# Kernel optimization log

Hardware: AMD Instinct MI355X
Metric: run time of the kernel (lower is better)

Reference implementation:

```python
import jax, jax.numpy as jnp
import numpy as np

H = 128          # hidden_size
D = 128          # input_size
N_LEAVES = 262144  # 2**18 leaves -> complete binary tree, 18 reduction levels


def setup_inputs() -> dict:
    key = jax.random.key(0)
    k1, k2, k3, k4, k5 = jax.random.split(key, 5)
    s = 0.05
    return {
        "leaf_features": jax.random.normal(k1, (N_LEAVES, D), jnp.float32),
        "W_x": jax.random.normal(k2, (D, 5 * H), jnp.float32) * s,  # torch Linear weight (transposed)
        "b_x": jax.random.normal(k3, (5 * H,), jnp.float32) * s,
        "U_L": jax.random.normal(k4, (H, 5 * H), jnp.float32) * s,  # no bias, per module
        "U_R": jax.random.normal(k5, (H, 5 * H), jnp.float32) * s,
    }


def _cell(gates, left_c=None, right_c=None):
    # gates: [n, 5H] -> chunk(5, dim=1) order: i, f_L, f_R, o, u
    i, f_L, f_R, o, u = jnp.split(gates, 5, axis=1)
    c = jax.nn.sigmoid(i) * jnp.tanh(u)
    if left_c is not None:
        c = c + jax.nn.sigmoid(f_L) * left_c
    if right_c is not None:
        c = c + jax.nn.sigmoid(f_R) * right_c
    h = jax.nn.sigmoid(o) * jnp.tanh(c)
    return h, c


def reference(leaf_features, W_x, b_x, U_L, U_R):
    # Leaves: cell(feat, None, None, None, None) -> only W_x gates, all nodes batched.
    h, c = _cell(leaf_features @ W_x + b_x)  # [N_LEAVES, H]
    # Internal nodes, processed level-by-level (depth batching of the recursion).
    # Internal x = zeros -> W_x contributes only its bias b_x.
    while h.shape[0] > 1:
        gates = b_x + h[0::2] @ U_L + h[1::2] @ U_R  # [n/2, 5H]
        h, c = _cell(gates, c[0::2], c[1::2])
    return h  # root hidden state, shape (1, H)
```

## Files before the change

### kernel.cpp

```cpp
#include <hip/hip_runtime.h>
#include <hip/hip_bf16.h>
#include <stdint.h>


#define H5 640
#define HH 128
#define NLEAF 262144

typedef __attribute__((ext_vector_type(4))) float f32x4;
typedef __attribute__((ext_vector_type(8))) short bf16x8;
typedef __attribute__((ext_vector_type(4))) unsigned int u32x4;

static __device__ __forceinline__ unsigned int f2bf(float f) {
  union { float f; unsigned int i; } v; v.f = f;
  unsigned int r = v.i + 0x7FFF + ((v.i >> 16) & 1);
  return r >> 16;
}

static __device__ __forceinline__ float sigf(float x) {
  return 1.0f / (1.0f + __expf(-x));
}
static __device__ __forceinline__ float tanh_fast(float x) {
  float t = __expf(2.0f * x);
  return (t - 1.0f) / (t + 1.0f);
}

__global__ void pack_weights(const float* __restrict__ srcA,
                             const float* __restrict__ srcB,
                             int split, int KT, unsigned short* __restrict__ dst) {
  int t = blockIdx.x * blockDim.x + threadIdx.x;
  int total = 40 * KT * 64;
  if (t >= total) return;
  int lane = t & 63;
  int kf = (t >> 6) % KT;
  int nf = (t >> 6) / KT;
  int col = nf * 16 + (lane & 15);
  int k0 = kf * 32 + (lane >> 4) * 8;
  unsigned int w[4];
#pragma unroll
  for (int p = 0; p < 4; ++p) {
    int ka = k0 + 2 * p, kb = k0 + 2 * p + 1;
    float fa = (ka < split) ? srcA[(size_t)ka * H5 + col] : srcB[(size_t)(ka - split) * H5 + col];
    float fb = (kb < split) ? srcA[(size_t)kb * H5 + col] : srcB[(size_t)(kb - split) * H5 + col];
    w[p] = f2bf(fa) | (f2bf(fb) << 16);
  }
  u32x4 v; unsigned int* vp = (unsigned int*)&v;
  vp[0] = w[0]; vp[1] = w[1]; vp[2] = w[2]; vp[3] = w[3];
  *((u32x4*)(dst + (size_t)t * 8)) = v;
}

template <int KT, bool LEAF>
__global__ __launch_bounds__(512, 4) void level_fused(
    const void* __restrict__ Araw,
    const unsigned short* __restrict__ Bpk,
    const float* __restrict__ bx,
    const float* __restrict__ c_child,
    unsigned short* __restrict__ h_out,
    float* __restrict__ c_out,
    float* __restrict__ h_f32_out,
    int n, int NT) {
  constexpr int K = KT * 32;
  __shared__ unsigned short smemB[5 * KT * 512];
  const int lane = threadIdx.x & 63;
  const int wid = threadIdx.x >> 6;
  const int by = blockIdx.y;

  {
    const int F = 5 * KT;
    for (int e = wid; e < F; e += 8) {
      int g = e / KT, kt = e % KT;
      const u32x4* src =
          (const u32x4*)(Bpk + ((size_t)((g * 8 + by) * KT + kt) * 512) + lane * 8);
      *((u32x4*)(smemB + e * 512 + lane * 8)) = *src;
    }
  }
  __syncthreads();

  const int jc = by * 16 + (lane & 15);
  float bxv[5];
#pragma unroll
  for (int g = 0; g < 5; ++g) bxv[g] = bx[g * 128 + jc];

  const unsigned short* Abf = (const unsigned short*)Araw;
  const float* Af = (const float*)Araw;
  const int kch = (lane >> 4) * 8;

  for (int t = blockIdx.x; t < NT; t += gridDim.x) {
    const int r0 = t * 256 + wid * 32 + (lane & 15);
    f32x4 acc[2][5];
#pragma unroll
    for (int m = 0; m < 2; ++m)
#pragma unroll
      for (int g = 0; g < 5; ++g) acc[m][g] = (f32x4)0.0f;

#pragma unroll 2
    for (int kt = 0; kt < KT; ++kt) {
      bf16x8 a[2];
      if (LEAF) {
#pragma unroll
        for (int m = 0; m < 2; ++m) {
          const float* p = Af + (size_t)(r0 + m * 16) * K + kt * 32 + kch;
          float4 x = *(const float4*)p;
          float4 y = *(const float4*)(p + 4);
          union { bf16x8 v; unsigned int u[4]; } w;
          w.u[0] = f2bf(x.x) | (f2bf(x.y) << 16);
          w.u[1] = f2bf(x.z) | (f2bf(x.w) << 16);
          w.u[2] = f2bf(y.x) | (f2bf(y.y) << 16);
          w.u[3] = f2bf(y.z) | (f2bf(y.w) << 16);
          a[m] = w.v;
        }
      } else {
#pragma unroll
        for (int m = 0; m < 2; ++m)
          a[m] = *(const bf16x8*)(Abf + (size_t)(r0 + m * 16) * K + kt * 32 + kch);
      }
#pragma unroll
      for (int g = 0; g < 5; ++g) {
        bf16x8 b = *(const bf16x8*)(smemB + (g * KT + kt) * 512 + lane * 8);
        acc[0][g] = __builtin_amdgcn_mfma_f32_16x16x32_bf16(a[0], b, acc[0][g], 0, 0, 0);
        acc[1][g] = __builtin_amdgcn_mfma_f32_16x16x32_bf16(a[1], b, acc[1][g], 0, 0, 0);
      }
    }

#pragma unroll
    for (int m = 0; m < 2; ++m) {
      const int ib = t * 256 + wid * 32 + m * 16 + (lane >> 4) * 4;
#pragma unroll
      for (int reg = 0; reg < 4; ++reg) {
        const int i = ib + reg;
        if (i >= n) continue;
        float gi = acc[m][0][reg] + bxv[0];
        float go = acc[m][3][reg] + bxv[3];
        float gu = acc[m][4][reg] + bxv[4];
        float c = sigf(gi) * tanh_fast(gu);
        if (!LEAF) {
          float gfL = acc[m][1][reg] + bxv[1];
          float gfR = acc[m][2][reg] + bxv[2];
          float cL = c_child[(size_t)(2 * i) * HH + jc];
          float cR = c_child[(size_t)(2 * i + 1) * HH + jc];
          c += sigf(gfL) * cL + sigf(gfR) * cR;
        }
        float h = sigf(go) * tanh_fast(c);
        h_out[(size_t)i * HH + jc] = (unsigned short)f2bf(h);
        c_out[(size_t)i * HH + jc] = c;
        if (h_f32_out) h_f32_out[(size_t)i * HH + jc] = h;
      }
    }
  }
}

extern "C" void kernel_launch(void* const* d_in, const int* in_sizes, int n_in,
                              void* d_out, int out_size, void* d_ws, size_t ws_size,
                              hipStream_t stream) {
  const float* leaf = (const float*)d_in[0];
  const float* Wx = (const float*)d_in[1];
  const float* bx = (const float*)d_in[2];
  const float* UL = (const float*)d_in[3];
  const float* UR = (const float*)d_in[4];
  float* out = (float*)d_out;

  char* ws = (char*)d_ws;
  size_t off = 0;
  auto alloc = [&](size_t bytes) -> void* {
    void* p = ws + off;
    off += (bytes + 1023) & ~(size_t)1023;
    return p;
  };
  unsigned short* Wx_pk = (unsigned short*)alloc((size_t)40 * 4 * 64 * 8 * 2);
  unsigned short* U_pk = (unsigned short*)alloc((size_t)40 * 8 * 64 * 8 * 2);
  unsigned short* hA = (unsigned short*)alloc((size_t)NLEAF * HH * 2);
  unsigned short* hB = (unsigned short*)alloc((size_t)(NLEAF / 2) * HH * 2);
  float* cA = (float*)alloc((size_t)NLEAF * HH * 4);
  float* cB = (float*)alloc((size_t)(NLEAF / 2) * HH * 4);

  pack_weights<<<(40 * 4 * 64 + 255) / 256, 256, 0, stream>>>(Wx, Wx, 128, 4, Wx_pk);
  pack_weights<<<(40 * 8 * 64 + 255) / 256, 256, 0, stream>>>(UL, UR, 128, 8, U_pk);

  {
    int NT = NLEAF / 256;
    int gx = 128;
    level_fused<4, true><<<dim3(gx, 8), 512, 0, stream>>>(
        leaf, Wx_pk, bx, nullptr, hA, cA, nullptr, NLEAF, NT);
  }

  unsigned short* hs[2] = {hA, hB};
  float* cs[2] = {cA, cB};
  int cur = 0;
  int n = NLEAF / 2;
  for (int lvl = 1; lvl <= 18; ++lvl) {
    unsigned short* hin = hs[cur];
    float* cin = cs[cur];
    unsigned short* hout = hs[cur ^ 1];
    float* cout = cs[cur ^ 1];
    float* f32out = (lvl == 18) ? out : nullptr;
    int NT = (n + 255) / 256;
    int gx = NT < 96 ? NT : 96;
    level_fused<8, false><<<dim3(gx, 8), 512, 0, stream>>>(
        hin, U_pk, bx, cin, hout, cout, f32out, n, NT);
    cur ^= 1;
    n >>= 1;
  }
  (void)in_sizes; (void)n_in; (void)out_size; (void)ws_size;
}
```

Measured before the change: 761.4 us.

## Fuse last ten tree levels into one persistent kernel with grid barriers

The last ten reduction levels now run in a single persistent kernel of 64 blocks, with atomic-counter grid barriers between levels, instead of ten separate tiny launches. This removes launch overhead and idle gaps on the small levels. Leaf features are also cast to bf16 in a separate pass before the leaf GEMM rather than converted inline, and the grid width of the per-level launches changes from 96 to 128. The extra cast pass adds a full read and write of the leaf data, and the spin barrier assumes all 64 blocks are resident at once.

```diff
diff --git a/kernel.cpp b/kernel.cpp
--- a/kernel.cpp
+++ b/kernel.cpp
@@ -49,9 +49,23 @@
   *((u32x4*)(dst + (size_t)t * 8)) = v;
 }
 
-template <int KT, bool LEAF>
+__global__ void cast_leaf(const float* __restrict__ src,
+                          unsigned short* __restrict__ dst, long n8) {
+  long t = (long)blockIdx.x * blockDim.x + threadIdx.x;
+  if (t >= n8) return;
+  const float4* s = (const float4*)src + t * 2;
+  float4 x = s[0], y = s[1];
+  u32x4 v; unsigned int* vp = (unsigned int*)&v;
+  vp[0] = f2bf(x.x) | (f2bf(x.y) << 16);
+  vp[1] = f2bf(x.z) | (f2bf(x.w) << 16);
+  vp[2] = f2bf(y.x) | (f2bf(y.y) << 16);
+  vp[3] = f2bf(y.z) | (f2bf(y.w) << 16);
+  *((u32x4*)(dst + t * 8)) = v;
+}
+
+template <int KT, bool HAS_C>
 __global__ __launch_bounds__(512, 4) void level_fused(
-    const void* __restrict__ Araw,
+    const unsigned short* __restrict__ A,
     const unsigned short* __restrict__ Bpk,
     const float* __restrict__ bx,
     const float* __restrict__ c_child,
@@ -65,14 +79,11 @@
   const int wid = threadIdx.x >> 6;
   const int by = blockIdx.y;
 
-  {
-    const int F = 5 * KT;
-    for (int e = wid; e < F; e += 8) {
-      int g = e / KT, kt = e % KT;
-      const u32x4* src =
-          (const u32x4*)(Bpk + ((size_t)((g * 8 + by) * KT + kt) * 512) + lane * 8);
-      *((u32x4*)(smemB + e * 512 + lane * 8)) = *src;
-    }
+  for (int e = wid; e < 5 * KT; e += 8) {
+    int g = e / KT, kt = e % KT;
+    const u32x4* src =
+        (const u32x4*)(Bpk + ((size_t)((g * 8 + by) * KT + kt) * 512) + lane * 8);
+    *((u32x4*)(smemB + e * 512 + lane * 8)) = *src;
   }
   __syncthreads();
 
@@ -81,8 +92,6 @@
 #pragma unroll
   for (int g = 0; g < 5; ++g) bxv[g] = bx[g * 128 + jc];
 
-  const unsigned short* Abf = (const unsigned short*)Araw;
-  const float* Af = (const float*)Araw;
   const int kch = (lane >> 4) * 8;
 
   for (int t = blockIdx.x; t < NT; t += gridDim.x) {
@@ -96,24 +105,9 @@
 #pragma unroll 2
     for (int kt = 0; kt < KT; ++kt) {
       bf16x8 a[2];
-      if (LEAF) {
-#pragma unroll
-        for (int m = 0; m < 2; ++m) {
-          const float* p = Af + (size_t)(r0 + m * 16) * K + kt * 32 + kch;
-          float4 x = *(const float4*)p;
-          float4 y = *(const float4*)(p + 4);
-          union { bf16x8 v; unsigned int u[4]; } w;
-          w.u[0] = f2bf(x.x) | (f2bf(x.y) << 16);
-          w.u[1] = f2bf(x.z) | (f2bf(x.w) << 16);
-          w.u[2] = f2bf(y.x) | (f2bf(y.y) << 16);
-          w.u[3] = f2bf(y.z) | (f2bf(y.w) << 16);
-          a[m] = w.v;
-        }
-      } else {
-#pragma unroll
-        for (int m = 0; m < 2; ++m)
-          a[m] = *(const bf16x8*)(Abf + (size_t)(r0 + m * 16) * K + kt * 32 + kch);
-      }
+#pragma unroll
+      for (int m = 0; m < 2; ++m)
+        a[m] = *(const bf16x8*)(A + (size_t)(r0 + m * 16) * K + kt * 32 + kch);
 #pragma unroll
       for (int g = 0; g < 5; ++g) {
         bf16x8 b = *(const bf16x8*)(smemB + (g * KT + kt) * 512 + lane * 8);
@@ -133,7 +127,7 @@
         float go = acc[m][3][reg] + bxv[3];
         float gu = acc[m][4][reg] + bxv[4];
         float c = sigf(gi) * tanh_fast(gu);
-        if (!LEAF) {
+        if (HAS_C) {
           float gfL = acc[m][1][reg] + bxv[1];
           float gfR = acc[m][2][reg] + bxv[2];
           float cL = c_child[(size_t)(2 * i) * HH + jc];
@@ -146,6 +140,110 @@
         if (h_f32_out) h_f32_out[(size_t)i * HH + jc] = h;
       }
     }
+  }
+}
+
+__global__ __launch_bounds__(512, 4) void tail_fused(
+    const unsigned short* __restrict__ h_in0,
+    const float* __restrict__ c_in0,
+    const unsigned short* __restrict__ Bpk,
+    const float* __restrict__ bx,
+    unsigned short* __restrict__ tailH,
+    float* __restrict__ tailC,
+    float* __restrict__ out,
+    int* __restrict__ bar) {
+  constexpr int KT = 8;
+  constexpr int K = 256;
+  __shared__ unsigned short smemB[5 * KT * 512];
+  const int lane = threadIdx.x & 63;
+  const int wid = threadIdx.x >> 6;
+  const int by = blockIdx.y;
+  const int bxk = blockIdx.x;
+
+  for (int e = wid; e < 5 * KT; e += 8) {
+    int g = e / KT, kt = e % KT;
+    const u32x4* src =
+        (const u32x4*)(Bpk + ((size_t)((g * 8 + by) * KT + kt) * 512) + lane * 8);
+    *((u32x4*)(smemB + e * 512 + lane * 8)) = *src;
+  }
+  __syncthreads();
+
+  const int jc = by * 16 + (lane & 15);
+  float bxv[5];
+#pragma unroll
+  for (int g = 0; g < 5; ++g) bxv[g] = bx[g * 128 + jc];
+  const int kch = (lane >> 4) * 8;
+
+  const unsigned short* hin = h_in0;
+  const float* cin = c_in0;
+  size_t off = 0;
+  int nout = 512;
+  for (int l = 0; l < 10; ++l, nout >>= 1) {
+    unsigned short* hout = tailH + off * HH;
+    float* cout = tailC + off * HH;
+    const int NT = (nout + 255) >> 8;
+    for (int t = bxk; t < NT; t += 8) {
+      const int r0 = t * 256 + wid * 32 + (lane & 15);
+      f32x4 acc[2][5];
+#pragma unroll
+      for (int m = 0; m < 2; ++m)
+#pragma unroll
+        for (int g = 0; g < 5; ++g) acc[m][g] = (f32x4)0.0f;
+
+      for (int kt = 0; kt < KT; ++kt) {
+        bf16x8 a[2];
+#pragma unroll
+        for (int m = 0; m < 2; ++m) {
+          int ar = r0 + m * 16;
+          if (ar >= nout) ar = 0;
+          a[m] = *(const bf16x8*)(hin + (size_t)ar * K + kt * 32 + kch);
+        }
+#pragma unroll
+        for (int g = 0; g < 5; ++g) {
+          bf16x8 b = *(const bf16x8*)(smemB + (g * KT + kt) * 512 + lane * 8);
+          acc[0][g] = __builtin_amdgcn_mfma_f32_16x16x32_bf16(a[0], b, acc[0][g], 0, 0, 0);
+          acc[1][g] = __builtin_amdgcn_mfma_f32_16x16x32_bf16(a[1], b, acc[1][g], 0, 0, 0);
+        }
+      }
+
+#pragma unroll
+      for (int m = 0; m < 2; ++m) {
+        const int ib = t * 256 + wid * 32 + m * 16 + (lane >> 4) * 4;
+#pragma unroll
+        for (int reg = 0; reg < 4; ++reg) {
+          const int i = ib + reg;
+          if (i >= nout) continue;
+          float gi = acc[m][0][reg] + bxv[0];
+          float go = acc[m][3][reg] + bxv[3];
+          float gu = acc[m][4][reg] + bxv[4];
+          float gfL = acc[m][1][reg] + bxv[1];
+          float gfR = acc[m][2][reg] + bxv[2];
+          float c = sigf(gi) * tanh_fast(gu) +
+                    sigf(gfL) * cin[(size_t)(2 * i) * HH + jc] +
+                    sigf(gfR) * cin[(size_t)(2 * i + 1) * HH + jc];
+          float h = sigf(go) * tanh_fast(c);
+          hout[(size_t)i * HH + jc] = (unsigned short)f2bf(h);
+          cout[(size_t)i * HH + jc] = c;
+          if (l == 9) out[jc] = h;
+        }
+      }
+    }
+
+    if (l < 9) {
+      __syncthreads();
+      if (threadIdx.x == 0) {
+        __threadfence();
+        atomicAdd(&bar[l], 1);
+        while (__hip_atomic_load(&bar[l], __ATOMIC_ACQUIRE,
+                                 __HIP_MEMORY_SCOPE_AGENT) < 64) {
+          __builtin_amdgcn_s_sleep(1);
+        }
+      }
+      __syncthreads();
+    }
+    hin = hout;
+    cin = cout;
+    off += nout;
   }
 }
 
@@ -168,37 +266,39 @@
   };
   unsigned short* Wx_pk = (unsigned short*)alloc((size_t)40 * 4 * 64 * 8 * 2);
   unsigned short* U_pk = (unsigned short*)alloc((size_t)40 * 8 * 64 * 8 * 2);
+  unsigned short* leaf_bf = (unsigned short*)alloc((size_t)NLEAF * HH * 2);
   unsigned short* hA = (unsigned short*)alloc((size_t)NLEAF * HH * 2);
   unsigned short* hB = (unsigned short*)alloc((size_t)(NLEAF / 2) * HH * 2);
   float* cA = (float*)alloc((size_t)NLEAF * HH * 4);
   float* cB = (float*)alloc((size_t)(NLEAF / 2) * HH * 4);
+  unsigned short* tailH = (unsigned short*)alloc((size_t)2048 * HH * 2);
+  float* tailC = (float*)alloc((size_t)2048 * HH * 4);
+  int* bar = (int*)alloc(64 * sizeof(int));
 
   pack_weights<<<(40 * 4 * 64 + 255) / 256, 256, 0, stream>>>(Wx, Wx, 128, 4, Wx_pk);
   pack_weights<<<(40 * 8 * 64 + 255) / 256, 256, 0, stream>>>(UL, UR, 128, 8, U_pk);
-
-  {
-    int NT = NLEAF / 256;
-    int gx = 128;
-    level_fused<4, true><<<dim3(gx, 8), 512, 0, stream>>>(
-        leaf, Wx_pk, bx, nullptr, hA, cA, nullptr, NLEAF, NT);
-  }
+  long n8 = (long)NLEAF * HH / 8;
+  cast_leaf<<<(unsigned)(n8 / 256), 256, 0, stream>>>(leaf, leaf_bf, n8);
+
+  level_fused<4, false><<<dim3(128, 8), 512, 0, stream>>>(
+      leaf_bf, Wx_pk, bx, nullptr, hA, cA, nullptr, NLEAF, NLEAF / 256);
 
   unsigned short* hs[2] = {hA, hB};
   float* cs[2] = {cA, cB};
   int cur = 0;
   int n = NLEAF / 2;
-  for (int lvl = 1; lvl <= 18; ++lvl) {
-    unsigned short* hin = hs[cur];
-    float* cin = cs[cur];
-    unsigned short* hout = hs[cur ^ 1];
-    float* cout = cs[cur ^ 1];
-    float* f32out = (lvl == 18) ? out : nullptr;
+  for (int lvl = 1; lvl <= 8; ++lvl) {
     int NT = (n + 255) / 256;
-    int gx = NT < 96 ? NT : 96;
-    level_fused<8, false><<<dim3(gx, 8), 512, 0, stream>>>(
-        hin, U_pk, bx, cin, hout, cout, f32out, n, NT);
+    int gx = NT < 128 ? NT : 128;
+    level_fused<8, true><<<dim3(gx, 8), 512, 0, stream>>>(
+        hs[cur], U_pk, bx, cs[cur], hs[cur ^ 1], cs[cur ^ 1], nullptr, n, NT);
     cur ^= 1;
     n >>= 1;
   }
+
+  hipMemsetAsync(bar, 0, 64 * sizeof(int), stream);
+  tail_fused<<<dim3(8, 8), 512, 0, stream>>>(
+      hs[cur], cs[cur], U_pk, bx, tailH, tailC, out, bar);
+
   (void)in_sizes; (void)n_in; (void)out_size; (void)ws_size;
 }
```

Result: slower. 826.2 us (+8.5%).

## Pre-cast leaves to bf16 and give each wave 64 rows with 256-thread blocks

Applied to the files above, without the earlier changes.

Adds a separate kernel that casts the fp32 leaf features to bf16 once, so the leaf GEMM reads bf16 like the internal levels. Blocks shrink from 512 to 256 threads, and each wave now computes four 16-row MFMA tiles instead of two. This raises reuse of each shared-memory B fragment per load and raises grid width for the internal levels. The cost is an extra leaf-sized round trip through memory and higher accumulator register pressure, which may lower occupancy.

```diff
diff --git a/kernel.cpp b/kernel.cpp
--- a/kernel.cpp
+++ b/kernel.cpp
@@ -49,9 +49,23 @@
   *((u32x4*)(dst + (size_t)t * 8)) = v;
 }
 
-template <int KT, bool LEAF>
-__global__ __launch_bounds__(512, 4) void level_fused(
-    const void* __restrict__ Araw,
+__global__ void cast_leaf(const float* __restrict__ src,
+                          unsigned short* __restrict__ dst, long n8) {
+  long t = (long)blockIdx.x * blockDim.x + threadIdx.x;
+  if (t >= n8) return;
+  const float4* s = (const float4*)src + t * 2;
+  float4 x = s[0], y = s[1];
+  u32x4 v; unsigned int* vp = (unsigned int*)&v;
+  vp[0] = f2bf(x.x) | (f2bf(x.y) << 16);
+  vp[1] = f2bf(x.z) | (f2bf(x.w) << 16);
+  vp[2] = f2bf(y.x) | (f2bf(y.y) << 16);
+  vp[3] = f2bf(y.z) | (f2bf(y.w) << 16);
+  *((u32x4*)(dst + t * 8)) = v;
+}
+
+template <int KT, bool HAS_C>
+__global__ __launch_bounds__(256, 4) void level_fused(
+    const unsigned short* __restrict__ A,
     const unsigned short* __restrict__ Bpk,
     const float* __restrict__ bx,
     const float* __restrict__ c_child,
@@ -65,14 +79,11 @@
   const int wid = threadIdx.x >> 6;
   const int by = blockIdx.y;
 
-  {
-    const int F = 5 * KT;
-    for (int e = wid; e < F; e += 8) {
-      int g = e / KT, kt = e % KT;
-      const u32x4* src =
-          (const u32x4*)(Bpk + ((size_t)((g * 8 + by) * KT + kt) * 512) + lane * 8);
-      *((u32x4*)(smemB + e * 512 + lane * 8)) = *src;
-    }
+  for (int e = wid; e < 5 * KT; e += 4) {
+    int g = e / KT, kt = e % KT;
+    const u32x4* src =
+        (const u32x4*)(Bpk + ((size_t)((g * 8 + by) * KT + kt) * 512) + lane * 8);
+    *((u32x4*)(smemB + e * 512 + lane * 8)) = *src;
   }
   __syncthreads();
 
@@ -81,50 +92,34 @@
 #pragma unroll
   for (int g = 0; g < 5; ++g) bxv[g] = bx[g * 128 + jc];
 
-  const unsigned short* Abf = (const unsigned short*)Araw;
-  const float* Af = (const float*)Araw;
   const int kch = (lane >> 4) * 8;
 
   for (int t = blockIdx.x; t < NT; t += gridDim.x) {
-    const int r0 = t * 256 + wid * 32 + (lane & 15);
-    f32x4 acc[2][5];
+    const int r0 = t * 256 + wid * 64 + (lane & 15);
+    f32x4 acc[4][5];
 #pragma unroll
-    for (int m = 0; m < 2; ++m)
+    for (int m = 0; m < 4; ++m)
 #pragma unroll
       for (int g = 0; g < 5; ++g) acc[m][g] = (f32x4)0.0f;
 
 #pragma unroll 2
     for (int kt = 0; kt < KT; ++kt) {
-      bf16x8 a[2];
-      if (LEAF) {
+      bf16x8 a[4];
 #pragma unroll
-        for (int m = 0; m < 2; ++m) {
-          const float* p = Af + (size_t)(r0 + m * 16) * K + kt * 32 + kch;
-          float4 x = *(const float4*)p;
-          float4 y = *(const float4*)(p + 4);
-          union { bf16x8 v; unsigned int u[4]; } w;
-          w.u[0] = f2bf(x.x) | (f2bf(x.y) << 16);
-          w.u[1] = f2bf(x.z) | (f2bf(x.w) << 16);
-          w.u[2] = f2bf(y.x) | (f2bf(y.y) << 16);
-          w.u[3] = f2bf(y.z) | (f2bf(y.w) << 16);
-          a[m] = w.v;
-        }
-      } else {
-#pragma unroll
-        for (int m = 0; m < 2; ++m)
-          a[m] = *(const bf16x8*)(Abf + (size_t)(r0 + m * 16) * K + kt * 32 + kch);
-      }
+      for (int m = 0; m < 4; ++m)
+        a[m] = *(const bf16x8*)(A + (size_t)(r0 + m * 16) * K + kt * 32 + kch);
 #pragma unroll
       for (int g = 0; g < 5; ++g) {
         bf16x8 b = *(const bf16x8*)(smemB + (g * KT + kt) * 512 + lane * 8);
-        acc[0][g] = __builtin_amdgcn_mfma_f32_16x16x32_bf16(a[0], b, acc[0][g], 0, 0, 0);
-        acc[1][g] = __builtin_amdgcn_mfma_f32_16x16x32_bf16(a[1], b, acc[1][g], 0, 0, 0);
+#pragma unroll
+        for (int m = 0; m < 4; ++m)
+          acc[m][g] = __builtin_amdgcn_mfma_f32_16x16x32_bf16(a[m], b, acc[m][g], 0, 0, 0);
       }
     }
 
 #pragma unroll
-    for (int m = 0; m < 2; ++m) {
-      const int ib = t * 256 + wid * 32 + m * 16 + (lane >> 4) * 4;
+    for (int m = 0; m < 4; ++m) {
+      const int ib = t * 256 + wid * 64 + m * 16 + (lane >> 4) * 4;
 #pragma unroll
       for (int reg = 0; reg < 4; ++reg) {
         const int i = ib + reg;
@@ -133,7 +128,7 @@
         float go = acc[m][3][reg] + bxv[3];
         float gu = acc[m][4][reg] + bxv[4];
         float c = sigf(gi) * tanh_fast(gu);
-        if (!LEAF) {
+        if (HAS_C) {
           float gfL = acc[m][1][reg] + bxv[1];
           float gfR = acc[m][2][reg] + bxv[2];
           float cL = c_child[(size_t)(2 * i) * HH + jc];
@@ -168,6 +163,7 @@
   };
   unsigned short* Wx_pk = (unsigned short*)alloc((size_t)40 * 4 * 64 * 8 * 2);
   unsigned short* U_pk = (unsigned short*)alloc((size_t)40 * 8 * 64 * 8 * 2);
+  unsigned short* leaf_bf = (unsigned short*)alloc((size_t)NLEAF * HH * 2);
   unsigned short* hA = (unsigned short*)alloc((size_t)NLEAF * HH * 2);
   unsigned short* hB = (unsigned short*)alloc((size_t)(NLEAF / 2) * HH * 2);
   float* cA = (float*)alloc((size_t)NLEAF * HH * 4);
@@ -175,28 +171,22 @@
 
   pack_weights<<<(40 * 4 * 64 + 255) / 256, 256, 0, stream>>>(Wx, Wx, 128, 4, Wx_pk);
   pack_weights<<<(40 * 8 * 64 + 255) / 256, 256, 0, stream>>>(UL, UR, 128, 8, U_pk);
+  long n8 = (long)NLEAF * HH / 8;
+  cast_leaf<<<(unsigned)(n8 / 256), 256, 0, stream>>>(leaf, leaf_bf, n8);
 
-  {
-    int NT = NLEAF / 256;
-    int gx = 128;
-    level_fused<4, true><<<dim3(gx, 8), 512, 0, stream>>>(
-        leaf, Wx_pk, bx, nullptr, hA, cA, nullptr, NLEAF, NT);
-  }
+  level_fused<4, false><<<dim3(128, 8), 256, 0, stream>>>(
+      leaf_bf, Wx_pk, bx, nullptr, hA, cA, nullptr, NLEAF, NLEAF / 256);
 
   unsigned short* hs[2] = {hA, hB};
   float* cs[2] = {cA, cB};
   int cur = 0;
   int n = NLEAF / 2;
   for (int lvl = 1; lvl <= 18; ++lvl) {
-    unsigned short* hin = hs[cur];
-    float* cin = cs[cur];
-    unsigned short* hout = hs[cur ^ 1];
-    float* cout = cs[cur ^ 1];
     float* f32out = (lvl == 18) ? out : nullptr;
     int NT = (n + 255) / 256;
-    int gx = NT < 96 ? NT : 96;
-    level_fused<8, false><<<dim3(gx, 8), 512, 0, stream>>>(
-        hin, U_pk, bx, cin, hout, cout, f32out, n, NT);
+    int gx = NT < 128 ? NT : 128;
+    level_fused<8, true><<<dim3(gx, 8), 256, 0, stream>>>(
+        hs[cur], U_pk, bx, cs[cur], hs[cur ^ 1], cs[cur ^ 1], f32out, n, NT);
     cur ^= 1;
     n >>= 1;
   }
```

Result: slower. 787.2 us (+3.4%).
